# Optimization experiments

Measured on AMD Instinct MI355X. Metric: run time of the kernel, lower is better.

Reference implementation:

```python
import jax, jax.numpy as jnp
import numpy as np

N_NODES = 50000
N_GRAPHS = 64
IN_DIM, HIDDEN, OUT_DIM = 2063, 256, 128
E_L, E_G = 800000, 1600000


def setup_inputs() -> dict:
    key = jax.random.key(0)
    ks = jax.random.split(key, 16)
    x = jax.random.normal(ks[0], (N_NODES, IN_DIM), dtype=jnp.float32)
    edge_index_l = jax.random.randint(ks[1], (2, E_L), 0, N_NODES, dtype=jnp.int64)
    edge_index_g = jax.random.randint(ks[2], (2, E_G), 0, N_NODES, dtype=jnp.int64)
    batch = jnp.sort(jax.random.randint(ks[3], (N_NODES,), 0, N_GRAPHS, dtype=jnp.int64))

    def glorot(k, shape):
        scale = jnp.sqrt(2.0 / (shape[0] + shape[1])).astype(jnp.float32)
        return jax.random.normal(k, shape, dtype=jnp.float32) * scale

    return {
        "x": x,
        "edge_index_l": edge_index_l,
        "edge_index_g": edge_index_g,
        "batch": batch,
        "W_l1": glorot(ks[4], (IN_DIM, HIDDEN)), "b_l1": jnp.zeros((HIDDEN,), jnp.float32),
        "W_l2": glorot(ks[5], (HIDDEN, OUT_DIM)), "b_l2": jnp.zeros((OUT_DIM,), jnp.float32),
        "W_g1": glorot(ks[6], (IN_DIM, HIDDEN)), "b_g1": jnp.zeros((HIDDEN,), jnp.float32),
        "W_g2": glorot(ks[7], (HIDDEN, OUT_DIM)), "b_g2": jnp.zeros((OUT_DIM,), jnp.float32),
        "W_fuse": glorot(ks[8], (2 * OUT_DIM, OUT_DIM)), "b_fuse": jnp.zeros((OUT_DIM,), jnp.float32),
    }


def gcn_conv(x, edge_index, W, b):
    # PyG GCNConv: add self loops, symmetric D^{-1/2}(A+I)D^{-1/2} normalization,
    # linear transform then scatter-add aggregation at target nodes.
    n = x.shape[0]
    loops = jnp.arange(n, dtype=edge_index.dtype)
    src = jnp.concatenate([edge_index[0], loops])
    dst = jnp.concatenate([edge_index[1], loops])
    deg = jax.ops.segment_sum(jnp.ones_like(dst, dtype=x.dtype), dst, num_segments=n)
    dinv = jax.lax.rsqrt(deg)  # deg >= 1 due to self loops
    norm = dinv[src] * dinv[dst]  # [E+n]
    h = x @ W  # [n, out]
    msg = h[src] * norm[:, None]  # gather + scale
    return jax.ops.segment_sum(msg, dst, num_segments=n) + b


def global_mean_pool(x, batch, num_graphs):
    sums = jax.ops.segment_sum(x, batch, num_segments=num_graphs)
    cnt = jax.ops.segment_sum(jnp.ones((x.shape[0],), x.dtype), batch, num_segments=num_graphs)
    return sums / jnp.maximum(cnt, 1.0)[:, None]


def reference(x, edge_index_l, edge_index_g, batch,
              W_l1, b_l1, W_l2, b_l2, W_g1, b_g1, W_g2, b_g2, W_fuse, b_fuse):
    # dropout is identity in eval mode
    xl = jax.nn.relu(gcn_conv(x, edge_index_l, W_l1, b_l1))
    xl = gcn_conv(xl, edge_index_l, W_l2, b_l2)
    xl = global_mean_pool(xl, batch, N_GRAPHS)

    xg = jax.nn.relu(gcn_conv(x, edge_index_g, W_g1, b_g1))
    xg = gcn_conv(xg, edge_index_g, W_g2, b_g2)
    xg = global_mean_pool(xg, batch, N_GRAPHS)

    out = jnp.concatenate([xl, xg], axis=1)  # [G, 2*out_dim]
    return jax.nn.relu(out @ W_fuse + b_fuse)
```

## Files before the change

### kernel.cpp

```cpp
#include <hip/hip_runtime.h>
#include <hip/hip_bf16.h>
#include <cstdint>
#include <cstddef>


#define N_NODES 50000
#define N_GRAPHS 64
#define IN_DIM 2063
#define HIDDEN 256
#define OUT_DIM 128
#define EDGES_L 800000
#define EDGES_G 1600000
#define HCOLS 512
#define KPAD 2112
#define MPAD 50048
#define GBM 64
#define NGB (MPAD / GBM)
#define NT (KPAD / 32)
#define PCH 256
#define NCHUNK ((N_NODES + PCH - 1) / PCH)

#define QUARTER 12544
#define SL_L 64
#define SL_G 128
#define EPS 12500
#define HBLOCKS (4 * (SL_L + SL_G))

typedef __attribute__((ext_vector_type(8))) __bf16 bf16x8;
typedef __attribute__((ext_vector_type(4))) float f32x4;

__device__ __forceinline__ float bf2f(unsigned short u) {
  union { unsigned int i; float f; } c; c.i = ((unsigned int)u) << 16; return c.f;
}
__device__ __forceinline__ unsigned short f2bf(float f) {
  __hip_bfloat16 h = __float2bfloat16(f);
  return *reinterpret_cast<unsigned short*>(&h);
}

__global__ void k_cvt_w(const float* __restrict__ Wl, const float* __restrict__ Wg,
                        unsigned short* __restrict__ Wt) {
  int i = blockIdx.x * blockDim.x + threadIdx.x;
  if (i >= HCOLS * KPAD) return;
  int n = i / KPAD;
  int k = i - n * KPAD;
  float v = 0.f;
  if (k < IN_DIM) {
    v = (n < HIDDEN) ? Wl[(size_t)k * HIDDEN + n] : Wg[(size_t)k * HIDDEN + (n - HIDDEN)];
  }
  Wt[(size_t)n * KPAD + k] = f2bf(v);
}

__launch_bounds__(256)
__global__ void k_hist(const int* __restrict__ dstL, const int* __restrict__ dstG,
                       int* __restrict__ partL, int* __restrict__ partG) {
  __shared__ int hist[QUARTER];
  const int i = blockIdx.x;
  const int* __restrict__ dst;
  int slice, q;
  int* __restrict__ part;
  if (i < 4 * SL_L) {
    slice = i >> 2; q = i & 3;
    dst = dstL;
    part = partL + (size_t)(slice * 4 + q) * QUARTER;
  } else {
    int j = i - 4 * SL_L;
    slice = j >> 2; q = j & 3;
    dst = dstG;
    part = partG + (size_t)(slice * 4 + q) * QUARTER;
  }
  for (int t = threadIdx.x; t < QUARTER; t += 256) hist[t] = 0;
  __syncthreads();
  const int e0 = slice * EPS;
  const int qbase = q * QUARTER;
  for (int e = e0 + threadIdx.x; e < e0 + EPS; e += 256) {
    int d = dst[e] - qbase;
    if ((unsigned)d < QUARTER) atomicAdd(&hist[d], 1);
  }
  __syncthreads();
  for (int t = threadIdx.x; t < QUARTER; t += 256) part[t] = hist[t];
}

__global__ void k_prefix(int* __restrict__ partL, int* __restrict__ partG,
                         const int* __restrict__ batch, int* __restrict__ degL,
                         int* __restrict__ degG, float* __restrict__ dinvL,
                         float* __restrict__ dinvG, float* __restrict__ cL,
                         float* __restrict__ cG) {
  int t = blockIdx.x * blockDim.x + threadIdx.x;
  if (t >= 8 * QUARTER) return;
  const int b = t / (4 * QUARTER);
  const int n = t - b * 4 * QUARTER;
  const int q = n / QUARTER, loc = n - q * QUARTER;
  const int NS = b ? SL_G : SL_L;
  int* p = (b ? partG : partL) + (size_t)q * QUARTER + loc;
  int run = 0;
  for (int s = 0; s < NS; s++) {
    int* pp = p + (size_t)s * 4 * QUARTER;
    int v = *pp;
    *pp = run;
    run += v;
  }
  if (n < N_NODES) {
    float d = 1.0f / sqrtf((float)(run + 1));
    if (b == 0) {
      degL[n] = run; dinvL[n] = d; cL[(size_t)n * 64 + batch[n]] = d * d;
    } else {
      degG[n] = run; dinvG[n] = d; cG[(size_t)n * 64 + batch[n]] = d * d;
    }
  }
}

__global__ void k_scan1(const int* __restrict__ degL, const int* __restrict__ degG,
                        int* __restrict__ rowL, int* __restrict__ rowG,
                        const int* __restrict__ batch, int* __restrict__ start) {
  if (blockIdx.x >= 2) {
    int n = (blockIdx.x - 2) * 1024 + threadIdx.x;
    if (n >= N_NODES) return;
    int bn = batch[n];
    int bp = n ? batch[n - 1] : -1;
    for (int g = bp + 1; g <= bn; g++) start[g] = n;
    if (n == N_NODES - 1)
      for (int g = bn + 1; g <= N_GRAPHS; g++) start[g] = N_NODES;
    return;
  }
  __shared__ int part[1024];
  const int t = threadIdx.x;
  const int* __restrict__ deg = blockIdx.x ? degG : degL;
  int* __restrict__ row = blockIdx.x ? rowG : rowL;
  const int c0 = t * 49;
  int s = 0;
  for (int j = 0; j < 49; j++) {
    int idx = c0 + j;
    s += (idx < N_NODES) ? deg[idx] : 0;
  }
  part[t] = s;
  __syncthreads();
  for (int ofs = 1; ofs < 1024; ofs <<= 1) {
    int v = (t >= ofs) ? part[t - ofs] : 0;
    __syncthreads();
    part[t] += v;
    __syncthreads();
  }
  int run = (t > 0) ? part[t - 1] : 0;
  for (int j = 0; j < 49; j++) {
    int idx = c0 + j;
    if (idx < N_NODES) { row[idx] = run; run += deg[idx]; }
  }
  if (t == 1023) row[N_NODES] = part[1023];
}

__launch_bounds__(256)
__global__ void k_gemm_scat(const float* __restrict__ X,
                            const unsigned short* __restrict__ Wt,
                            unsigned short* __restrict__ H,
                            const int* __restrict__ srcL, const int* __restrict__ dstL,
                            const int* __restrict__ srcG, const int* __restrict__ dstG,
                            const int* __restrict__ partL, const int* __restrict__ partG,
                            const int* __restrict__ rowL, const int* __restrict__ rowG,
                            const float* __restrict__ dinvL, const float* __restrict__ dinvG,
                            const int* __restrict__ batch, int2* __restrict__ erL,
                            int2* __restrict__ erG, float* __restrict__ cL,
                            float* __restrict__ cG) {
  __shared__ __align__(16) char lds[2 * 4096 + 2 * 32768];

  if (blockIdx.x >= NGB) {
    int* hist = (int*)lds;
    const int i = blockIdx.x - NGB;
    const int *src, *dst, *part, *row;
    const float* dinv;
    int2* er;
    float* c;
    int slice, q;
    if (i < 4 * SL_L) {
      slice = i >> 2; q = i & 3;
      src = srcL; dst = dstL; row = rowL; dinv = dinvL; er = erL; c = cL;
      part = partL + (size_t)(slice * 4 + q) * QUARTER;
    } else {
      int j = i - 4 * SL_L;
      slice = j >> 2; q = j & 3;
      src = srcG; dst = dstG; row = rowG; dinv = dinvG; er = erG; c = cG;
      part = partG + (size_t)(slice * 4 + q) * QUARTER;
    }
    for (int t = threadIdx.x; t < QUARTER; t += 256) hist[t] = 0;
    __syncthreads();
    const int e0 = slice * EPS;
    const int qbase = q * QUARTER;
    for (int e = e0 + threadIdx.x; e < e0 + EPS; e += 256) {
      int d = dst[e];
      int loc = d - qbase;
      if ((unsigned)loc < QUARTER) {
        int s = src[e];
        int rank = atomicAdd(&hist[loc], 1);
        int pos = row[d] + part[loc] + rank;
        float nrm = dinv[s] * dinv[d];
        er[pos] = make_int2(s, __float_as_int(nrm));
        atomicAdd(&c[(size_t)s * 64 + batch[d]], nrm);
      }
    }
    return;
  }

  char* const Ab0 = lds;
  char* const Ab1 = lds + 4096;
  char* const Bb0 = lds + 8192;
  char* const Bb1 = lds + 8192 + 32768;
  const int tid = threadIdx.x;
  const int lane = tid & 63;
  const int wave = tid >> 6;
  const int brow = blockIdx.x * GBM;

  const int ar = tid >> 2;
  const int ach = tid & 3;
  const int askew = (ar >> 1) & 3;
  const int asrc = (ach ^ askew) * 8;
  const int arow_g = brow + ar;
  const bool aok = arow_g < N_NODES;
  const float* __restrict__ Arow = X + (size_t)arow_g * IN_DIM;

  const int fr = lane & 15;
  const int fq = lane >> 4;

  f32x4 acc[4][8];
  const f32x4 zero = {0.f, 0.f, 0.f, 0.f};
#pragma unroll
  for (int m = 0; m < 4; m++)
#pragma unroll
    for (int n = 0; n < 8; n++) acc[m][n] = zero;

#pragma unroll
  for (int i = 0; i < 8; i++) {
    const int s = i * 256 + tid;
    const int row = s >> 2, cch = s & 3;
    const unsigned short* g = Wt + (size_t)row * KPAD + ((cch ^ ((row >> 1) & 3)) * 8);
    __builtin_amdgcn_global_load_lds(
        (const __attribute__((address_space(1))) void*)g,
        (__attribute__((address_space(3))) void*)(Bb0 + (i * 256 + wave * 64) * 16),
        16, 0, 0);
  }
  float a[8];
#pragma unroll
  for (int j = 0; j < 8; j++) a[j] = aok ? Arow[asrc + j] : 0.f;
  {
    uint u0 = (uint)f2bf(a[0]) | ((uint)f2bf(a[1]) << 16);
    uint u1 = (uint)f2bf(a[2]) | ((uint)f2bf(a[3]) << 16);
    uint u2 = (uint)f2bf(a[4]) | ((uint)f2bf(a[5]) << 16);
    uint u3 = (uint)f2bf(a[6]) | ((uint)f2bf(a[7]) << 16);
    *(uint4*)(Ab0 + tid * 16) = make_uint4(u0, u1, u2, u3);
  }
  __syncthreads();

  for (int t = 0; t < NT; ++t) {
    const int k0 = t * 32;
    char* const Acur = (t & 1) ? Ab1 : Ab0;
    char* const Bcur = (t & 1) ? Bb1 : Bb0;
    char* const Anxt = (t & 1) ? Ab0 : Ab1;
    char* const Bnxt = (t & 1) ? Bb0 : Bb1;

    if (t + 1 < NT) {
      const int kn = k0 + 32;
#pragma unroll
      for (int i = 0; i < 8; i++) {
        const int s = i * 256 + tid;
        const int row = s >> 2, cch = s & 3;
        const unsigned short* g = Wt + (size_t)row * KPAD + kn + ((cch ^ ((row >> 1) & 3)) * 8);
        __builtin_amdgcn_global_load_lds(
            (const __attribute__((address_space(1))) void*)g,
            (__attribute__((address_space(3))) void*)(Bnxt + (i * 256 + wave * 64) * 16),
            16, 0, 0);
      }
      const int kb = kn + asrc;
      if (aok) {
        if (kb + 7 < IN_DIM) {
#pragma unroll
          for (int j = 0; j < 8; j++) a[j] = Arow[kb + j];
        } else {
#pragma unroll
          for (int j = 0; j < 8; j++) a[j] = (kb + j < IN_DIM) ? Arow[kb + j] : 0.f;
        }
      }
    }

    {
      bf16x8 bv[8];
#pragma unroll
      for (int n = 0; n < 8; n++) {
        const int row = wave * 128 + n * 16 + fr;
        bv[n] = *(const bf16x8*)(Bcur + row * 64 + ((fq ^ ((row >> 1) & 3)) * 16));
      }
#pragma unroll
      for (int m = 0; m < 4; m++) {
        const int row = m * 16 + fr;
        bf16x8 av = *(const bf16x8*)(Acur + row * 64 + ((fq ^ ((row >> 1) & 3)) * 16));
#pragma unroll
        for (int n = 0; n < 8; n++)
          acc[m][n] = __builtin_amdgcn_mfma_f32_16x16x32_bf16(av, bv[n], acc[m][n], 0, 0, 0);
      }
    }

    if (t + 1 < NT) {
      uint u0 = (uint)f2bf(a[0]) | ((uint)f2bf(a[1]) << 16);
      uint u1 = (uint)f2bf(a[2]) | ((uint)f2bf(a[3]) << 16);
      uint u2 = (uint)f2bf(a[4]) | ((uint)f2bf(a[5]) << 16);
      uint u3 = (uint)f2bf(a[6]) | ((uint)f2bf(a[7]) << 16);
      *(uint4*)(Anxt + tid * 16) = make_uint4(u0, u1, u2, u3);
    }
    __syncthreads();
  }

#pragma unroll
  for (int m = 0; m < 4; m++) {
    const int r0 = brow + m * 16 + fq * 4;
#pragma unroll
    for (int n = 0; n < 8; n++) {
      const int col = wave * 128 + n * 16 + fr;
#pragma unroll
      for (int j = 0; j < 4; j++) {
        int r = r0 + j;
        if (r < N_NODES) H[(size_t)r * HCOLS + col] = f2bf(acc[m][n][j]);
      }
    }
  }
}

__global__ void k_agg(const unsigned short* __restrict__ h,
                      const float* __restrict__ dinvL, const float* __restrict__ dinvG,
                      const int* __restrict__ rowL, const int* __restrict__ rowG,
                      const int2* __restrict__ erL, const int2* __restrict__ erG,
                      const float* __restrict__ biasL, const float* __restrict__ biasG,
                      unsigned short* __restrict__ xl) {
  const int br = blockIdx.y;
  const int node = blockIdx.x * 4 + (threadIdx.x >> 6);
  const int lane = threadIdx.x & 63;
  const float* __restrict__ dinv = br ? dinvG : dinvL;
  const int* __restrict__ rp = br ? rowG : rowL;
  const int2* __restrict__ er = br ? erG : erL;
  const float* __restrict__ bias = br ? biasG : biasL;
  const int off = br ? 256 : 0;
  const size_t lcol = off + lane * 4;

  float di = dinv[node];
  float w0 = di * di;
  ushort4 u = *(const ushort4*)(h + (size_t)node * HCOLS + lcol);
  float a0 = w0 * bf2f(u.x), a1 = w0 * bf2f(u.y), a2 = w0 * bf2f(u.z), a3 = w0 * bf2f(u.w);

  int e = rp[node];
  const int e1 = rp[node + 1];
  for (; e + 8 <= e1; e += 8) {
    int2 r[8];
    ushort4 v[8];
#pragma unroll
    for (int j = 0; j < 8; j++) r[j] = er[e + j];
#pragma unroll
    for (int j = 0; j < 8; j++)
      v[j] = *(const ushort4*)(h + (size_t)r[j].x * HCOLS + lcol);
#pragma unroll
    for (int j = 0; j < 8; j++) {
      float w = __int_as_float(r[j].y);
      a0 = fmaf(w, bf2f(v[j].x), a0);
      a1 = fmaf(w, bf2f(v[j].y), a1);
      a2 = fmaf(w, bf2f(v[j].z), a2);
      a3 = fmaf(w, bf2f(v[j].w), a3);
    }
  }
  for (; e + 4 <= e1; e += 4) {
    int2 r[4];
    ushort4 v[4];
#pragma unroll
    for (int j = 0; j < 4; j++) r[j] = er[e + j];
#pragma unroll
    for (int j = 0; j < 4; j++)
      v[j] = *(const ushort4*)(h + (size_t)r[j].x * HCOLS + lcol);
#pragma unroll
    for (int j = 0; j < 4; j++) {
      float w = __int_as_float(r[j].y);
      a0 = fmaf(w, bf2f(v[j].x), a0);
      a1 = fmaf(w, bf2f(v[j].y), a1);
      a2 = fmaf(w, bf2f(v[j].z), a2);
      a3 = fmaf(w, bf2f(v[j].w), a3);
    }
  }
  for (; e < e1; e++) {
    int2 r = er[e];
    float w = __int_as_float(r.y);
    ushort4 v = *(const ushort4*)(h + (size_t)r.x * HCOLS + lcol);
    a0 = fmaf(w, bf2f(v.x), a0);
    a1 = fmaf(w, bf2f(v.y), a1);
    a2 = fmaf(w, bf2f(v.z), a2);
    a3 = fmaf(w, bf2f(v.w), a3);
  }
  float4 b = *(const float4*)(bias + lane * 4);
  ushort4 o;
  o.x = f2bf(fmaxf(a0 + b.x, 0.f));
  o.y = f2bf(fmaxf(a1 + b.y, 0.f));
  o.z = f2bf(fmaxf(a2 + b.z, 0.f));
  o.w = f2bf(fmaxf(a3 + b.w, 0.f));
  *(ushort4*)(xl + (size_t)node * HCOLS + lcol) = o;
}

__launch_bounds__(256)
__global__ void k_pool2(const unsigned short* __restrict__ xl,
                        const float* __restrict__ cL, const float* __restrict__ cG,
                        float* __restrict__ Spart) {
  __shared__ float cs[64][64];
  const int t = threadIdx.x;
  const int chunk = blockIdx.x;
  const int br = blockIdx.y;
  const float* __restrict__ C = br ? cG : cL;
  const int xoff = br ? 256 : 0;
  const int n0 = chunk * PCH;
  float acc[64];
#pragma unroll
  for (int g = 0; g < 64; g++) acc[g] = 0.f;

  for (int tile = 0; tile < PCH; tile += 64) {
    const int base = n0 + tile;
    __syncthreads();
#pragma unroll
    for (int i = 0; i < 16; i++) {
      int idx = i * 256 + t;
      int nn = idx >> 6, gg = idx & 63;
      int node = base + nn;
      cs[nn][gg] = (node < N_NODES) ? C[(size_t)node * 64 + gg] : 0.f;
    }
    __syncthreads();
    for (int nn = 0; nn < 64; nn++) {
      int node = base + nn;
      float v = (node < N_NODES) ? bf2f(xl[(size_t)node * HCOLS + xoff + t]) : 0.f;
#pragma unroll
      for (int g4 = 0; g4 < 16; g4++) {
        float4 cv = *(const float4*)&cs[nn][g4 * 4];
        acc[g4 * 4 + 0] = fmaf(cv.x, v, acc[g4 * 4 + 0]);
        acc[g4 * 4 + 1] = fmaf(cv.y, v, acc[g4 * 4 + 1]);
        acc[g4 * 4 + 2] = fmaf(cv.z, v, acc[g4 * 4 + 2]);
        acc[g4 * 4 + 3] = fmaf(cv.w, v, acc[g4 * 4 + 3]);
      }
    }
  }
  float* sp = Spart + ((size_t)br * NCHUNK + chunk) * 16384 + t;
#pragma unroll
  for (int g = 0; g < 64; g++) sp[g * 256] = acc[g];
}

__global__ void k_pool_reduce(const float* __restrict__ Spart, float* __restrict__ S) {
  int i = blockIdx.x * blockDim.x + threadIdx.x;
  if (i >= 2 * 16384) return;
  int br = i >> 14, idx = i & 16383;
  const float* p = Spart + (size_t)br * NCHUNK * 16384 + idx;
  float s = 0.f;
  for (int ch = 0; ch < NCHUNK; ch++) s += p[(size_t)ch * 16384];
  S[i] = s;
}

__global__ void k_final(const float* __restrict__ S,
                        const float* __restrict__ Wl2, const float* __restrict__ bl2,
                        const float* __restrict__ Wg2, const float* __restrict__ bg2,
                        const float* __restrict__ Wf, const float* __restrict__ bf,
                        const int* __restrict__ start, float* __restrict__ out) {
  __shared__ float pl[OUT_DIM], pg[OUT_DIM];
  int g = blockIdx.x, t = threadIdx.x;
  float invc = 1.0f / fmaxf((float)(start[g + 1] - start[g]), 1.0f);
  const float* Sl = S + (size_t)g * HIDDEN;
  const float* Sg = S + (size_t)N_GRAPHS * HIDDEN + (size_t)g * HIDDEN;
  float al = 0.f, ag = 0.f;
  for (int k = 0; k < HIDDEN; k++) {
    al = fmaf(Sl[k], Wl2[k * OUT_DIM + t], al);
    ag = fmaf(Sg[k], Wg2[k * OUT_DIM + t], ag);
  }
  pl[t] = al * invc + bl2[t];
  pg[t] = ag * invc + bg2[t];
  __syncthreads();
  float o = bf[t];
  for (int j = 0; j < OUT_DIM; j++) {
    o = fmaf(pl[j], Wf[j * OUT_DIM + t], o);
    o = fmaf(pg[j], Wf[(OUT_DIM + j) * OUT_DIM + t], o);
  }
  out[(size_t)g * OUT_DIM + t] = fmaxf(o, 0.f);
}

extern "C" void kernel_launch(void* const* d_in, const int* in_sizes, int n_in,
                              void* d_out, int out_size, void* d_ws, size_t ws_size,
                              hipStream_t stream) {
  const float* x = (const float*)d_in[0];
  const int* el = (const int*)d_in[1];
  const int* eg = (const int*)d_in[2];
  const int* batch = (const int*)d_in[3];
  const float* Wl1 = (const float*)d_in[4];
  const float* bl1 = (const float*)d_in[5];
  const float* Wl2 = (const float*)d_in[6];
  const float* bl2 = (const float*)d_in[7];
  const float* Wg1 = (const float*)d_in[8];
  const float* bg1 = (const float*)d_in[9];
  const float* Wg2 = (const float*)d_in[10];
  const float* bg2 = (const float*)d_in[11];
  const float* Wf = (const float*)d_in[12];
  const float* bf = (const float*)d_in[13];
  float* out = (float*)d_out;
  char* ws = (char*)d_ws;

  const size_t NPAD = 200192;
  size_t off = 0;
  float* c_l = (float*)(ws + off); off += (size_t)N_NODES * 64 * 4;
  float* c_g = (float*)(ws + off); off += (size_t)N_NODES * 64 * 4;
  const size_t zero_bytes = off;
  int* start = (int*)(ws + off); off += 512;
  float* S = (float*)(ws + off); off += (size_t)2 * N_GRAPHS * HIDDEN * 4;
  int* deg_l = (int*)(ws + off); off += NPAD;
  int* deg_g = (int*)(ws + off); off += NPAD;
  float* dinv_l = (float*)(ws + off); off += NPAD;
  float* dinv_g = (float*)(ws + off); off += NPAD;
  int* row_l = (int*)(ws + off); off += NPAD;
  int* row_g = (int*)(ws + off); off += NPAD;
  int* partL = (int*)(ws + off); off += (size_t)SL_L * 4 * QUARTER * 4;
  int* partG = (int*)(ws + off); off += (size_t)SL_G * 4 * QUARTER * 4;
  int2* er_l = (int2*)(ws + off); off += (size_t)EDGES_L * 8;
  int2* er_g = (int2*)(ws + off); off += (size_t)EDGES_G * 8;
  unsigned short* Wt = (unsigned short*)(ws + off); off += (size_t)HCOLS * KPAD * 2;
  unsigned short* h = (unsigned short*)(ws + off); off += (size_t)N_NODES * HCOLS * 2;
  unsigned short* xl = (unsigned short*)(ws + off); off += (size_t)N_NODES * HCOLS * 2;
  float* Spart = (float*)partL;

  const int* srcL = el;
  const int* dstL = el + EDGES_L;
  const int* srcG = eg;
  const int* dstG = eg + EDGES_G;

  hipMemsetAsync(ws, 0, zero_bytes, stream);

  k_cvt_w<<<(HCOLS * KPAD + 255) / 256, 256, 0, stream>>>(Wl1, Wg1, Wt);

  k_hist<<<HBLOCKS, 256, 0, stream>>>(dstL, dstG, partL, partG);
  k_prefix<<<(8 * QUARTER + 255) / 256, 256, 0, stream>>>(partL, partG, batch, deg_l, deg_g,
                                                          dinv_l, dinv_g, c_l, c_g);
  k_scan1<<<51, 1024, 0, stream>>>(deg_l, deg_g, row_l, row_g, batch, start);

  k_gemm_scat<<<NGB + HBLOCKS, 256, 0, stream>>>(x, Wt, h, srcL, dstL, srcG, dstG,
                                                 partL, partG, row_l, row_g, dinv_l, dinv_g,
                                                 batch, er_l, er_g, c_l, c_g);

  dim3 agrid(N_NODES / 4, 2);
  k_agg<<<agrid, 256, 0, stream>>>(h, dinv_l, dinv_g, row_l, row_g, er_l, er_g, bl1, bg1, xl);

  dim3 pgrid(NCHUNK, 2);
  k_pool2<<<pgrid, 256, 0, stream>>>(xl, c_l, c_g, Spart);
  k_pool_reduce<<<(2 * 16384 + 255) / 256, 256, 0, stream>>>(Spart, S);

  k_final<<<N_GRAPHS, OUT_DIM, 0, stream>>>(S, Wl2, bl2, Wg2, bg2, Wf, bf, start, out);
}
```

Measured before the change: 935.6 us.

## Store first-layer GEMM output in FP8 and gather FP8 rows in aggregation

The GEMM epilogue now writes the hidden features H as FP8 bytes instead of bf16, and the aggregation kernel gathers 4-byte FP8 packs per lane and converts them with hardware cvt instructions. This halves the bytes moved by the random-gather aggregation and the GEMM store. The aggregation inner loop is unrolled from 8 to 16 edges for more loads in flight, and MFMA sections get raised wave priority via s_setprio. The cost is a large precision loss (FP8 mantissa) on intermediate activations, which may violate tolerance, plus higher register pressure from the deeper unroll.

```diff
diff --git a/kernel.cpp b/kernel.cpp
--- a/kernel.cpp
+++ b/kernel.cpp
@@ -35,6 +35,9 @@
 __device__ __forceinline__ unsigned short f2bf(float f) {
   __hip_bfloat16 h = __float2bfloat16(f);
   return *reinterpret_cast<unsigned short*>(&h);
+}
+__device__ __forceinline__ unsigned char f2fp8(float f) {
+  return (unsigned char)(__builtin_amdgcn_cvt_pk_fp8_f32(f, f, 0, 0) & 0xff);
 }
 
 __global__ void k_cvt_w(const float* __restrict__ Wl, const float* __restrict__ Wg,
@@ -151,7 +154,7 @@
 __launch_bounds__(256)
 __global__ void k_gemm_scat(const float* __restrict__ X,
                             const unsigned short* __restrict__ Wt,
-                            unsigned short* __restrict__ H,
+                            unsigned char* __restrict__ H,
                             const int* __restrict__ srcL, const int* __restrict__ dstL,
                             const int* __restrict__ srcG, const int* __restrict__ dstG,
                             const int* __restrict__ partL, const int* __restrict__ partG,
@@ -280,6 +283,7 @@
     }
 
     {
+      __builtin_amdgcn_s_setprio(1);
       bf16x8 bv[8];
 #pragma unroll
       for (int n = 0; n < 8; n++) {
@@ -294,6 +298,7 @@
         for (int n = 0; n < 8; n++)
           acc[m][n] = __builtin_amdgcn_mfma_f32_16x16x32_bf16(av, bv[n], acc[m][n], 0, 0, 0);
       }
+      __builtin_amdgcn_s_setprio(0);
     }
 
     if (t + 1 < NT) {
@@ -315,13 +320,13 @@
 #pragma unroll
       for (int j = 0; j < 4; j++) {
         int r = r0 + j;
-        if (r < N_NODES) H[(size_t)r * HCOLS + col] = f2bf(acc[m][n][j]);
-      }
-    }
-  }
-}
-
-__global__ void k_agg(const unsigned short* __restrict__ h,
+        if (r < N_NODES) H[(size_t)r * HCOLS + col] = f2fp8(acc[m][n][j]);
+      }
+    }
+  }
+}
+
+__global__ void k_agg(const unsigned char* __restrict__ h,
                       const float* __restrict__ dinvL, const float* __restrict__ dinvG,
                       const int* __restrict__ rowL, const int* __restrict__ rowG,
                       const int2* __restrict__ erL, const int2* __restrict__ erG,
@@ -339,53 +344,56 @@
 
   float di = dinv[node];
   float w0 = di * di;
-  ushort4 u = *(const ushort4*)(h + (size_t)node * HCOLS + lcol);
-  float a0 = w0 * bf2f(u.x), a1 = w0 * bf2f(u.y), a2 = w0 * bf2f(u.z), a3 = w0 * bf2f(u.w);
+  uint u = *(const uint*)(h + (size_t)node * HCOLS + lcol);
+  float a0 = w0 * __builtin_amdgcn_cvt_f32_fp8(u, 0);
+  float a1 = w0 * __builtin_amdgcn_cvt_f32_fp8(u, 1);
+  float a2 = w0 * __builtin_amdgcn_cvt_f32_fp8(u, 2);
+  float a3 = w0 * __builtin_amdgcn_cvt_f32_fp8(u, 3);
 
   int e = rp[node];
   const int e1 = rp[node + 1];
-  for (; e + 8 <= e1; e += 8) {
-    int2 r[8];
-    ushort4 v[8];
-#pragma unroll
-    for (int j = 0; j < 8; j++) r[j] = er[e + j];
-#pragma unroll
-    for (int j = 0; j < 8; j++)
-      v[j] = *(const ushort4*)(h + (size_t)r[j].x * HCOLS + lcol);
-#pragma unroll
-    for (int j = 0; j < 8; j++) {
+  for (; e + 16 <= e1; e += 16) {
+    int2 r[16];
+    uint v[16];
+#pragma unroll
+    for (int j = 0; j < 16; j++) r[j] = er[e + j];
+#pragma unroll
+    for (int j = 0; j < 16; j++)
+      v[j] = *(const uint*)(h + (size_t)r[j].x * HCOLS + lcol);
+#pragma unroll
+    for (int j = 0; j < 16; j++) {
       float w = __int_as_float(r[j].y);
-      a0 = fmaf(w, bf2f(v[j].x), a0);
-      a1 = fmaf(w, bf2f(v[j].y), a1);
-      a2 = fmaf(w, bf2f(v[j].z), a2);
-      a3 = fmaf(w, bf2f(v[j].w), a3);
+      a0 = fmaf(w, __builtin_amdgcn_cvt_f32_fp8(v[j], 0), a0);
+      a1 = fmaf(w, __builtin_amdgcn_cvt_f32_fp8(v[j], 1), a1);
+      a2 = fmaf(w, __builtin_amdgcn_cvt_f32_fp8(v[j], 2), a2);
+      a3 = fmaf(w, __builtin_amdgcn_cvt_f32_fp8(v[j], 3), a3);
     }
   }
   for (; e + 4 <= e1; e += 4) {
     int2 r[4];
-    ushort4 v[4];
+    uint v[4];
 #pragma unroll
     for (int j = 0; j < 4; j++) r[j] = er[e + j];
 #pragma unroll
     for (int j = 0; j < 4; j++)
-      v[j] = *(const ushort4*)(h + (size_t)r[j].x * HCOLS + lcol);
+      v[j] = *(const uint*)(h + (size_t)r[j].x * HCOLS + lcol);
 #pragma unroll
     for (int j = 0; j < 4; j++) {
       float w = __int_as_float(r[j].y);
-      a0 = fmaf(w, bf2f(v[j].x), a0);
-      a1 = fmaf(w, bf2f(v[j].y), a1);
-      a2 = fmaf(w, bf2f(v[j].z), a2);
-      a3 = fmaf(w, bf2f(v[j].w), a3);
+      a0 = fmaf(w, __builtin_amdgcn_cvt_f32_fp8(v[j], 0), a0);
+      a1 = fmaf(w, __builtin_amdgcn_cvt_f32_fp8(v[j], 1), a1);
+      a2 = fmaf(w, __builtin_amdgcn_cvt_f32_fp8(v[j], 2), a2);
+      a3 = fmaf(w, __builtin_amdgcn_cvt_f32_fp8(v[j], 3), a3);
     }
   }
   for (; e < e1; e++) {
     int2 r = er[e];
     float w = __int_as_float(r.y);
-    ushort4 v = *(const ushort4*)(h + (size_t)r.x * HCOLS + lcol);
-    a0 = fmaf(w, bf2f(v.x), a0);
-    a1 = fmaf(w, bf2f(v.y), a1);
-    a2 = fmaf(w, bf2f(v.z), a2);
-    a3 = fmaf(w, bf2f(v.w), a3);
+    uint v = *(const uint*)(h + (size_t)r.x * HCOLS + lcol);
+    a0 = fmaf(w, __builtin_amdgcn_cvt_f32_fp8(v, 0), a0);
+    a1 = fmaf(w, __builtin_amdgcn_cvt_f32_fp8(v, 1), a1);
+    a2 = fmaf(w, __builtin_amdgcn_cvt_f32_fp8(v, 2), a2);
+    a3 = fmaf(w, __builtin_amdgcn_cvt_f32_fp8(v, 3), a3);
   }
   float4 b = *(const float4*)(bias + lane * 4);
   ushort4 o;
@@ -514,7 +522,7 @@
   int2* er_l = (int2*)(ws + off); off += (size_t)EDGES_L * 8;
   int2* er_g = (int2*)(ws + off); off += (size_t)EDGES_G * 8;
   unsigned short* Wt = (unsigned short*)(ws + off); off += (size_t)HCOLS * KPAD * 2;
-  unsigned short* h = (unsigned short*)(ws + off); off += (size_t)N_NODES * HCOLS * 2;
+  unsigned char* h = (unsigned char*)(ws + off); off += (size_t)N_NODES * HCOLS;
   unsigned short* xl = (unsigned short*)(ws + off); off += (size_t)N_NODES * HCOLS * 2;
   float* Spart = (float*)partL;
 
```

Measured after the change: 862.1 us. -7.8%, faster.
